# Kernel tuning notes

Measured on AMD Instinct MI355X. Metric: run time of the kernel, lower is better.

Reference implementation:

```python
import jax, jax.numpy as jnp
import numpy as np
import math

L_SIDE = 32           # one_side_length = ceil(sqrt(L)), L = 32**2
NDIM = 16             # args.ndim (SSM state size)
N_SSM = 16            # args.n_ssm
DIRS = 4              # args.directions_amount
EMBED = 1024          # embed_dim
KD = DIRS * N_SSM     # kernel_dim = 64
CDIM = EMBED * DIRS   # C_dimensions = 4096
H = EMBED // N_SSM    # 64 (channels per ssm)
R2 = 16               # expansion terms per kernel position
R = L_SIDE * L_SIDE * R2
V = 2 * L_SIDE        # vander power dim (power_dim = kernel_dim_arg*2)
BSZ = 8
SEQ = L_SIDE * L_SIDE


def _build_one_matrix():
    # Mimics CoeffCalculator.whole_as_one: for each of d=2 flow axes and each
    # of R expansion terms, the 4 A-factor rows are one-hot selectors over the
    # V power basis, and the 5th (B) row holds an integer coefficient in one of
    # the first two columns (selecting B1 or B2).
    rng = np.random.default_rng(0)
    M = np.zeros((2, 5, R, V), dtype=np.float32)
    di = np.arange(2)[:, None]
    ri = np.arange(R)[None, :]
    for a in range(4):
        idx = rng.integers(0, V, size=(2, R))
        M[di, a, ri, idx] = 1.0
    col = rng.integers(0, 2, size=(2, R))
    coef = rng.integers(1, 5, size=(2, R)).astype(np.float32)
    M[di, 4, ri, col] = coef
    return jnp.asarray(M)


def setup_inputs() -> dict:
    key = jax.random.key(0)
    ks = jax.random.split(key, 7)
    return {
        "x": jax.random.normal(ks[0], (SEQ, BSZ, EMBED), jnp.float32),
        "A": jax.random.normal(ks[1], (4, KD, NDIM), jnp.float32) * 0.2,
        "B1": jax.random.normal(ks[2], (KD, NDIM), jnp.float32) * 0.2,
        "B2": jax.random.normal(ks[3], (KD, NDIM), jnp.float32) * 0.2,
        "C1": jax.random.normal(ks[4], (CDIM, NDIM), jnp.float32),
        "C2": jax.random.normal(ks[5], (CDIM, NDIM), jnp.float32),
        "omega": jax.random.normal(ks[6], (EMBED,), jnp.float32),
        "one_matrix": _build_one_matrix(),
    }


def _compute_kernel(A, B1, B2, C1, C2, one_matrix, dtype):
    scale = 1.0 / math.sqrt(NDIM)
    # _calc_coeffs: sigmoid on A, B
    As = jax.nn.sigmoid(A)                                  # (4, KD, NDIM)
    pw = jnp.arange(V, dtype=dtype)
    # torch.linalg.vander: increasing powers 0..V-1 -> (4, V, KD, NDIM)
    A_vals = jnp.transpose(As[..., None] ** pw, (0, 3, 1, 2))
    Bs = jax.nn.sigmoid(jnp.stack([B1, B2], 0))             # (2, KD, NDIM)
    Bpad = jnp.zeros((V, KD, NDIM), dtype).at[:2].set(Bs)   # pad to V rows
    vals = jnp.concatenate([A_vals, Bpad[None]], 0)         # (5, V, KD, NDIM)
    # 'd a R V, a V k n -> d a R k n' then product over the 5 factors
    prod = jnp.einsum('drv,vkn->drkn', one_matrix[:, 0], vals[0])
    for a in range(1, 5):
        prod = prod * jnp.einsum('drv,vkn->drkn', one_matrix[:, a], vals[a])
    # sum over r2 expansion terms per kernel position
    w = prod.reshape(2, SEQ, R2, KD, NDIM).sum(2)           # (2, SEQ, KD, NDIM)
    C = jnp.stack([C1, C2], 0) * scale                      # (2, CDIM, NDIM)
    Cr = C.reshape(2, H, KD, NDIM)
    k = jnp.einsum('dpkn,dhkn->phk', w, Cr).reshape(L_SIDE, L_SIDE, CDIM)
    # boundary scaling (first row/col x2, corner net x1)
    k = k.at[0, :, :].multiply(2.0)
    k = k.at[:, 0, :].multiply(2.0)
    k = k.at[0, 0, :].divide(4.0)
    return k


def reference(x, A, B1, B2, C1, C2, omega, one_matrix):
    k = _compute_kernel(A, B1, B2, C1, C2, one_matrix, x.dtype)
    # channel layout (H, dir, n_ssm) -> per-direction (EMBED,) kernels
    kd = k.reshape(L_SIDE, L_SIDE, H, DIRS, N_SSM)
    kd = jnp.transpose(kd, (3, 2, 4, 0, 1)).reshape(DIRS, EMBED, L_SIDE, L_SIDE)
    # 4-corner scans: flip kernel per direction; conv is linear so sum kernels
    ksum = kd[0] + kd[1, :, ::-1, :] + kd[2, :, :, ::-1] + kd[3, :, ::-1, ::-1]
    residual = x * omega                                    # 'L B D, D -> L B D'
    xg = jnp.transpose(x, (1, 2, 0)).reshape(BSZ, EMBED, L_SIDE, L_SIDE)
    s = 2 * L_SIDE
    xf = jnp.fft.rfft2(xg, s=(s, s))                        # (B, D, s, s//2+1)
    kf = jnp.fft.rfft2(ksum, s=(s, s))
    y = jnp.fft.irfft2(xf * kf, s=(s, s))[..., :L_SIDE, :L_SIDE]
    y = jnp.transpose(y.reshape(BSZ, EMBED, SEQ), (2, 0, 1))  # back to (L, B, D)
    return y + residual
```

## Files before the change

### kernel.cpp

```cpp
#include <hip/hip_runtime.h>
#include <stdint.h>


typedef __attribute__((ext_vector_type(8))) short short8;
typedef __attribute__((ext_vector_type(4))) float f32x4;

__device__ inline uint16_t f2bf(float f) {
    uint32_t u = __float_as_uint(f);
    uint32_t r = (u + 0x7FFFu + ((u >> 16) & 1u)) >> 16;
    return (uint16_t)r;
}
__device__ inline float bf2f(uint16_t v) {
    return __uint_as_float((uint32_t)v << 16);
}
__device__ inline uint32_t packbf(float a, float b) {
    return (uint32_t)f2bf(a) | ((uint32_t)f2bf(b) << 16);
}

__global__ __launch_bounds__(256) void k_sel(const float* __restrict__ om,
                                             uint32_t* __restrict__ sel,
                                             float* __restrict__ coef) {
    int gw = (blockIdx.x * 256 + threadIdx.x) >> 6;
    int lane = threadIdx.x & 63;
    int nw = gridDim.x * 4;
    for (int pr = gw; pr < 32768; pr += nw) {
        int d = pr >> 14, r = pr & 16383;
        uint32_t s = 0;
        float cf = 1.0f;
        #pragma unroll
        for (int a = 0; a < 5; ++a) {
            float v = om[((size_t)(d * 5 + a) * 16384 + r) * 64 + lane];
            unsigned long long m = __ballot(v != 0.0f);
            int idx = (m != 0ull) ? __builtin_ctzll(m) : 0;
            float mv = __shfl(v, idx, 64);
            if (m == 0ull) mv = 0.0f;
            if (a < 4) {
                s |= (uint32_t)idx << (6 * a);
                cf *= mv;
            } else {
                if (idx > 1) cf = 0.0f;
                else { s |= (uint32_t)idx << 24; cf *= mv; }
            }
        }
        if (lane == 0) { sel[pr] = s; coef[pr] = cf; }
    }
}

__global__ __launch_bounds__(256) void k_w(const float* __restrict__ A,
                                           const float* __restrict__ B1,
                                           const float* __restrict__ B2,
                                           const uint32_t* __restrict__ sel,
                                           const float* __restrict__ coef,
                                           float* __restrict__ w) {
    int p = blockIdx.x;
    int t = threadIdx.x;
    int d = __builtin_amdgcn_readfirstlane(t >> 7);
    int j0 = (t & 127) * 8;

    float L0[8], L1[8], L2[8], L3[8], B0v[8], B1v[8], acc[8];
    {
        #pragma unroll
        for (int a = 0; a < 4; ++a) {
            float* La = (a == 0) ? L0 : (a == 1) ? L1 : (a == 2) ? L2 : L3;
            float4 u0 = *(const float4*)(A + a * 1024 + j0);
            float4 u1 = *(const float4*)(A + a * 1024 + j0 + 4);
            float tmp[8] = {u0.x, u0.y, u0.z, u0.w, u1.x, u1.y, u1.z, u1.w};
            #pragma unroll
            for (int jj = 0; jj < 8; ++jj)
                La[jj] = -log2f(1.0f + expf(-tmp[jj]));
        }
        float4 u0 = *(const float4*)(B1 + j0);
        float4 u1 = *(const float4*)(B1 + j0 + 4);
        float4 v0 = *(const float4*)(B2 + j0);
        float4 v1 = *(const float4*)(B2 + j0 + 4);
        float t1[8] = {u0.x, u0.y, u0.z, u0.w, u1.x, u1.y, u1.z, u1.w};
        float t2[8] = {v0.x, v0.y, v0.z, v0.w, v1.x, v1.y, v1.z, v1.w};
        #pragma unroll
        for (int jj = 0; jj < 8; ++jj) {
            B0v[jj] = 1.0f / (1.0f + expf(-t1[jj]));
            B1v[jj] = 1.0f / (1.0f + expf(-t2[jj]));
        }
    }
    #pragma unroll
    for (int jj = 0; jj < 8; ++jj) acc[jj] = 0.0f;

    int base = d * 16384 + p * 16;
    #pragma unroll
    for (int r2 = 0; r2 < 16; ++r2) {
        uint32_t s = sel[base + r2];
        float cf = coef[base + r2];
        float f0 = (float)(s & 63u);
        float f1 = (float)((s >> 6) & 63u);
        float f2 = (float)((s >> 12) & 63u);
        float f3 = (float)((s >> 18) & 63u);
        int col = (int)((s >> 24) & 1u);
        float c0 = col ? 0.0f : cf;
        float c1 = col ? cf : 0.0f;
        #pragma unroll
        for (int jj = 0; jj < 8; ++jj) {
            float ex = __builtin_fmaf(f3, L3[jj],
                       __builtin_fmaf(f2, L2[jj],
                       __builtin_fmaf(f1, L1[jj], f0 * L0[jj])));
            float bs = __builtin_fmaf(c1, B1v[jj], c0 * B0v[jj]);
            acc[jj] = __builtin_fmaf(exp2f(ex), bs, acc[jj]);
        }
    }
    float* dst = w + (size_t)(d * 1024 + p) * 1024 + j0;
    *(float4*)(dst)     = make_float4(acc[0], acc[1], acc[2], acc[3]);
    *(float4*)(dst + 4) = make_float4(acc[4], acc[5], acc[6], acc[7]);
}

__global__ __launch_bounds__(256) void k_kd(const float* __restrict__ w,
                                            const float* __restrict__ C1,
                                            const float* __restrict__ C2,
                                            uint16_t* __restrict__ kd4b) {
    __shared__ float Wl[128 * 33];
    __shared__ float Ctl[32 * 65];
    int kap = blockIdx.x;
    int p0 = blockIdx.y * 128;
    int dir = kap >> 4, m = kap & 15;
    int t = threadIdx.x;

    {
        int d = t >> 7, pp = t & 127;
        const float* src = w + ((size_t)(d * 1024 + p0 + pp) * 64 + kap) * 16;
        float* dst = Wl + pp * 33 + d * 16;
        #pragma unroll
        for (int q = 0; q < 4; ++q) {
            float4 v = *(const float4*)(src + q * 4);
            dst[q * 4 + 0] = v.x; dst[q * 4 + 1] = v.y;
            dst[q * 4 + 2] = v.z; dst[q * 4 + 3] = v.w;
        }
    }
    if (t < 128) {
        int d = t >> 6, h = t & 63;
        const float* Cd = d ? C2 : C1;
        const float* src = Cd + (size_t)(h * 64 + kap) * 16;
        #pragma unroll
        for (int q = 0; q < 16; ++q)
            Ctl[(d * 16 + q) * 65 + h] = src[q] * 0.25f;
    }
    __syncthreads();

    int ph = t & 15, hq = t >> 4;
    int pl = ph * 8, h0 = hq * 4;
    float acc[8][4];
    #pragma unroll
    for (int i = 0; i < 8; ++i)
        { acc[i][0] = acc[i][1] = acc[i][2] = acc[i][3] = 0.0f; }

    for (int k = 0; k < 32; ++k) {
        float c0 = Ctl[k * 65 + h0 + 0];
        float c1 = Ctl[k * 65 + h0 + 1];
        float c2 = Ctl[k * 65 + h0 + 2];
        float c3 = Ctl[k * 65 + h0 + 3];
        #pragma unroll
        for (int i = 0; i < 8; ++i) {
            float wv = Wl[(pl + i) * 33 + k];
            acc[i][0] += wv * c0; acc[i][1] += wv * c1;
            acc[i][2] += wv * c2; acc[i][3] += wv * c3;
        }
    }
    #pragma unroll
    for (int j = 0; j < 4; ++j) {
        int h = h0 + j;
        uint32_t pk[4];
        #pragma unroll
        for (int qq = 0; qq < 4; ++qq) {
            float v0, v1;
            #pragma unroll
            for (int z = 0; z < 2; ++z) {
                int p = p0 + pl + qq * 2 + z;
                int ii = p >> 5, jj = p & 31;
                float f = ((ii == 0) != (jj == 0)) ? 2.0f : 1.0f;
                float val = acc[qq * 2 + z][j] * f;
                if (z == 0) v0 = val; else v1 = val;
            }
            pk[qq] = packbf(v0, v1);
        }
        uint16_t* dst = kd4b + ((size_t)(dir * 1024 + h * 16 + m)) * 1024 + p0 + pl;
        *(uint4*)dst = make_uint4(pk[0], pk[1], pk[2], pk[3]);
    }
}

__global__ __launch_bounds__(256) void k_t1(const float* __restrict__ x,
                                            uint16_t* __restrict__ xtb) {
    __shared__ float lds[32 * 257];
    int u = blockIdx.x, e0 = blockIdx.y * 32;
    int t = threadIdx.x;
    {
        const float* src = x + (size_t)(u * 256 + t) * 1024 + e0;
        #pragma unroll
        for (int qq = 0; qq < 8; ++qq) {
            float4 v = *(const float4*)(src + qq * 4);
            lds[(qq * 4 + 0) * 257 + t] = v.x;
            lds[(qq * 4 + 1) * 257 + t] = v.y;
            lds[(qq * 4 + 2) * 257 + t] = v.z;
            lds[(qq * 4 + 3) * 257 + t] = v.w;
        }
    }
    __syncthreads();
    int er = t & 31, b = t >> 5;
    const float* row = lds + er * 257 + b;
    uint32_t pk[16];
    #pragma unroll
    for (int k2 = 0; k2 < 16; ++k2)
        pk[k2] = packbf(row[(2 * k2) * 8], row[(2 * k2 + 1) * 8]);
    uint16_t* dst = xtb + (size_t)(e0 + er) * 8192 + u * 256 + b * 32;
    uint4* d4 = (uint4*)dst;
    d4[0] = make_uint4(pk[0], pk[1], pk[2], pk[3]);
    d4[1] = make_uint4(pk[4], pk[5], pk[6], pk[7]);
    d4[2] = make_uint4(pk[8], pk[9], pk[10], pk[11]);
    d4[3] = make_uint4(pk[12], pk[13], pk[14], pk[15]);
}

__global__ __launch_bounds__(256) void k_conv(const uint16_t* __restrict__ xtb,
                                              const uint16_t* __restrict__ kd4b,
                                              uint16_t* __restrict__ ytb) {
    __shared__ __align__(16) char smem[26624 + 16384];
    const int KROW = 832;
    const int SROW = 104;
    char* xtl = smem + 26624;

    int e = blockIdx.x;
    int t = threadIdx.x;
    int lane = t & 63, wv = t >> 6;
    int n = lane & 15, q = lane >> 4, nn = n & 7;

    {
        f32x4 z = {0.f, 0.f, 0.f, 0.f};
        for (int idx = t; idx < 1664; idx += 256)
            *(f32x4*)(smem + idx * 16) = z;
    }
    {
        const uint4* src = (const uint4*)(xtb + (size_t)e * 8192);
        #pragma unroll
        for (int r = 0; r < 4; ++r) {
            uint4 v = src[r * 256 + t];
            *(uint4*)(xtl + (r * 256 + t) * 16) = v;
        }
    }
    int pi = t >> 3, pj = (t & 7) * 4;
    float s0, s1, s2, s3;
    {
        const uint16_t* b0 = kd4b + (size_t)e * 1024;
        ushort4 a0 = *(const ushort4*)(b0 + pi * 32 + pj);
        ushort4 a1 = *(const ushort4*)(b0 + (1 << 20) + (31 - pi) * 32 + pj);
        ushort4 a2 = *(const ushort4*)(b0 + (2 << 20) + pi * 32 + (28 - pj));
        ushort4 a3 = *(const ushort4*)(b0 + (3 << 20) + (31 - pi) * 32 + (28 - pj));
        s0 = bf2f(a0.x) + bf2f(a1.x) + bf2f(a2.w) + bf2f(a3.w);
        s1 = bf2f(a0.y) + bf2f(a1.y) + bf2f(a2.z) + bf2f(a3.z);
        s2 = bf2f(a0.z) + bf2f(a1.z) + bf2f(a2.y) + bf2f(a3.y);
        s3 = bf2f(a0.w) + bf2f(a1.w) + bf2f(a2.x) + bf2f(a3.x);
    }
    __syncthreads();

    {
        uint16_t k0 = f2bf(s0), k1 = f2bf(s1), k2 = f2bf(s2), k3 = f2bf(s3);
        #pragma unroll
        for (int s = 0; s < 8; ++s) {
            uint16_t* row = (uint16_t*)(smem + pi * KROW + s * SROW);
            int c = 31 + s - pj;
            row[c]     = k0;
            row[c - 1] = k1;
            row[c - 2] = k2;
            row[c - 3] = k3;
        }
    }
    __syncthreads();

    int A0 = n - 8 * q;
    int A1 = A0 + 16;
    int sh1 = (A1 + 9) & 7;
    int off1 = sh1 * SROW + (31 + sh1 - A1) * 2;
    int off0;
    if (A0 >= -8) {
        int sh0 = (A0 + 9) & 7;
        off0 = sh0 * SROW + (31 + sh0 - A0) * 2;
    } else {
        off0 = 80;
    }
    int boff = nn * 64 + q * 16;

    short8 Breg[16];
    #pragma unroll
    for (int u = 0; u < 16; ++u)
        Breg[u] = *(const short8*)(xtl + u * 512 + boff);

    f32x4 acc0[8], acc1[8];
    #pragma unroll
    for (int ii = 0; ii < 8; ++ii) {
        acc0[ii] = (f32x4){0.f, 0.f, 0.f, 0.f};
        acc1[ii] = (f32x4){0.f, 0.f, 0.f, 0.f};
    }

    #pragma unroll
    for (int dd = 0; dd < 4; ++dd) {
        if (dd <= wv) {
            const char* krow = smem + (wv - dd) * KROW;
            short8 a0 = *(const short8*)(krow + off0);
            short8 a1 = *(const short8*)(krow + off1);
            #pragma unroll
            for (int ii = 0; ii < 8; ++ii) {
                short8 bb = (ii < 4) ? Breg[dd + 4 * ii]
                                     : *(const short8*)(xtl + (dd + 4 * ii) * 512 + boff);
                acc0[ii] = __builtin_amdgcn_mfma_f32_16x16x32_bf16(a0, bb, acc0[ii], 0, 0, 0);
                acc1[ii] = __builtin_amdgcn_mfma_f32_16x16x32_bf16(a1, bb, acc1[ii], 0, 0, 0);
            }
        }
    }
    #pragma unroll
    for (int g = 1; g <= 7; ++g) {
        #pragma unroll
        for (int dd = 0; dd < 4; ++dd) {
            const char* krow = smem + (wv + 4 * g - 3 + dd) * KROW;
            short8 a0 = *(const short8*)(krow + off0);
            short8 a1 = *(const short8*)(krow + off1);
            #pragma unroll
            for (int ii = g; ii < 8; ++ii) {
                int u = 4 * (ii - g) + 3 - dd;
                short8 bb = (ii - g < 4) ? Breg[u]
                                         : *(const short8*)(xtl + u * 512 + boff);
                acc0[ii] = __builtin_amdgcn_mfma_f32_16x16x32_bf16(a0, bb, acc0[ii], 0, 0, 0);
                acc1[ii] = __builtin_amdgcn_mfma_f32_16x16x32_bf16(a1, bb, acc1[ii], 0, 0, 0);
            }
        }
    }

    if (n < 8) {
        uint16_t* base = ytb + ((size_t)(n * 1024 + e)) * 1024 + q * 4;
        #pragma unroll
        for (int ii = 0; ii < 8; ++ii) {
            int i = wv + 4 * ii;
            uint2 w0 = make_uint2(packbf(acc0[ii][0], acc0[ii][1]),
                                  packbf(acc0[ii][2], acc0[ii][3]));
            uint2 w1 = make_uint2(packbf(acc1[ii][0], acc1[ii][1]),
                                  packbf(acc1[ii][2], acc1[ii][3]));
            *(uint2*)(base + i * 32)      = w0;
            *(uint2*)(base + i * 32 + 16) = w1;
        }
    }
}

__global__ __launch_bounds__(256) void k_t2(const uint16_t* __restrict__ ytb,
                                            const float* __restrict__ x,
                                            const float* __restrict__ omega,
                                            float* __restrict__ out) {
    __shared__ float lds[32 * 129];
    int e0 = blockIdx.x * 32, p0 = blockIdx.y * 128, b = blockIdx.z;
    int t = threadIdx.x;
    {
        int er = t & 31, seg = t >> 5;
        const uint16_t* src = ytb + (size_t)(b * 1024 + e0 + er) * 1024 + p0 + seg * 16;
        uint4 v0 = *(const uint4*)src;
        uint4 v1 = *(const uint4*)(src + 8);
        float* dst = lds + er * 129 + seg * 16;
        uint32_t ww[8] = {v0.x, v0.y, v0.z, v0.w, v1.x, v1.y, v1.z, v1.w};
        #pragma unroll
        for (int k = 0; k < 8; ++k) {
            dst[2 * k]     = bf2f((uint16_t)(ww[k] & 0xFFFFu));
            dst[2 * k + 1] = bf2f((uint16_t)(ww[k] >> 16));
        }
    }
    __syncthreads();
    int pl = t >> 1, eh = (t & 1) * 16;
    int p = p0 + pl;
    const float* xs = x + ((size_t)(p * 8 + b)) * 1024 + e0 + eh;
    float* os = out + ((size_t)(p * 8 + b)) * 1024 + e0 + eh;
    #pragma unroll
    for (int qq = 0; qq < 4; ++qq) {
        float4 xv = *(const float4*)(xs + qq * 4);
        int eb = eh + qq * 4;
        float4 ov;
        ov.x = lds[(eb + 0) * 129 + pl] + xv.x * omega[e0 + eb + 0];
        ov.y = lds[(eb + 1) * 129 + pl] + xv.y * omega[e0 + eb + 1];
        ov.z = lds[(eb + 2) * 129 + pl] + xv.z * omega[e0 + eb + 2];
        ov.w = lds[(eb + 3) * 129 + pl] + xv.w * omega[e0 + eb + 3];
        *(float4*)(os + qq * 4) = ov;
    }
}

extern "C" void kernel_launch(void* const* d_in, const int* in_sizes, int n_in,
                              void* d_out, int out_size, void* d_ws, size_t ws_size,
                              hipStream_t stream) {
    (void)in_sizes; (void)n_in; (void)out_size; (void)ws_size;
    const float* x   = (const float*)d_in[0];
    const float* A   = (const float*)d_in[1];
    const float* B1  = (const float*)d_in[2];
    const float* B2  = (const float*)d_in[3];
    const float* C1  = (const float*)d_in[4];
    const float* C2  = (const float*)d_in[5];
    const float* omg = (const float*)d_in[6];
    const float* om  = (const float*)d_in[7];
    float* out = (float*)d_out;

    float* ws  = (float*)d_ws;
    uint16_t* xtb  = (uint16_t*)ws;
    uint16_t* kd4b = (uint16_t*)(ws + 4194304);
    uint16_t* ytb  = (uint16_t*)(ws + 6291456);
    uint32_t* sel  = (uint32_t*)(ws + 10485760);
    float* coef    = (float*)(sel + 32768);
    float* w       = coef + 32768;

    k_t1  <<<dim3(32, 32), 256, 0, stream>>>(x, xtb);
    k_sel <<<2048, 256, 0, stream>>>(om, sel, coef);
    k_w   <<<1024, 256, 0, stream>>>(A, B1, B2, sel, coef, w);
    k_kd  <<<dim3(64, 8), 256, 0, stream>>>(w, C1, C2, kd4b);
    k_conv<<<1024, 256, 0, stream>>>(xtb, kd4b, ytb);
    k_t2  <<<dim3(32, 8, 8), 256, 0, stream>>>(ytb, x, omg, out);
}
```

Before: 220.5 us.

## Fuse x transpose, selector extraction and w computation into one front kernel

Merges three kernels (x transpose to bf16, one-hot selector decoding, and w expansion) into a single launch. Block indices select which role each block takes. Selector and coefficient values now stay in shared memory instead of making a global round trip. k_conv's shared-memory row padding is also shrunk from 832 to 768 bytes, with an unrolled zero-fill. This removes two launches and the sel/coef global traffic, and lets the independent transpose overlap with the w computation. The smaller padding may bring back LDS bank conflicts, or may change the conv's layout assumptions.

Result: faster. 197.9 us (-10.2%).

```diff
diff --git a/kernel.cpp b/kernel.cpp
--- a/kernel.cpp
+++ b/kernel.cpp
@@ -17,48 +17,78 @@
     return (uint32_t)f2bf(a) | ((uint32_t)f2bf(b) << 16);
 }
 
-__global__ __launch_bounds__(256) void k_sel(const float* __restrict__ om,
-                                             uint32_t* __restrict__ sel,
-                                             float* __restrict__ coef) {
-    int gw = (blockIdx.x * 256 + threadIdx.x) >> 6;
-    int lane = threadIdx.x & 63;
-    int nw = gridDim.x * 4;
-    for (int pr = gw; pr < 32768; pr += nw) {
-        int d = pr >> 14, r = pr & 16383;
-        uint32_t s = 0;
-        float cf = 1.0f;
-        #pragma unroll
-        for (int a = 0; a < 5; ++a) {
-            float v = om[((size_t)(d * 5 + a) * 16384 + r) * 64 + lane];
-            unsigned long long m = __ballot(v != 0.0f);
-            int idx = (m != 0ull) ? __builtin_ctzll(m) : 0;
-            float mv = __shfl(v, idx, 64);
-            if (m == 0ull) mv = 0.0f;
-            if (a < 4) {
-                s |= (uint32_t)idx << (6 * a);
-                cf *= mv;
-            } else {
-                if (idx > 1) cf = 0.0f;
-                else { s |= (uint32_t)idx << 24; cf *= mv; }
-            }
-        }
-        if (lane == 0) { sel[pr] = s; coef[pr] = cf; }
-    }
-}
-
-__global__ __launch_bounds__(256) void k_w(const float* __restrict__ A,
-                                           const float* __restrict__ B1,
-                                           const float* __restrict__ B2,
-                                           const uint32_t* __restrict__ sel,
-                                           const float* __restrict__ coef,
-                                           float* __restrict__ w) {
-    int p = blockIdx.x;
+__global__ __launch_bounds__(256) void k_front(const float* __restrict__ x,
+                                               uint16_t* __restrict__ xtb,
+                                               const float* __restrict__ om,
+                                               const float* __restrict__ A,
+                                               const float* __restrict__ B1,
+                                               const float* __restrict__ B2,
+                                               float* __restrict__ w) {
+    __shared__ __align__(16) float shf[32 * 257];
+    int bx = blockIdx.x;
     int t = threadIdx.x;
-    int d = __builtin_amdgcn_readfirstlane(t >> 7);
-    int j0 = (t & 127) * 8;
-
-    float L0[8], L1[8], L2[8], L3[8], B0v[8], B1v[8], acc[8];
-    {
+
+    if (bx < 1024) {
+        int u = bx & 31, e0 = (bx >> 5) * 32;
+        {
+            const float* src = x + (size_t)(u * 256 + t) * 1024 + e0;
+            #pragma unroll
+            for (int qq = 0; qq < 8; ++qq) {
+                float4 v = *(const float4*)(src + qq * 4);
+                shf[(qq * 4 + 0) * 257 + t] = v.x;
+                shf[(qq * 4 + 1) * 257 + t] = v.y;
+                shf[(qq * 4 + 2) * 257 + t] = v.z;
+                shf[(qq * 4 + 3) * 257 + t] = v.w;
+            }
+        }
+        __syncthreads();
+        int er = t & 31, b = t >> 5;
+        const float* row = shf + er * 257 + b;
+        uint32_t pk[16];
+        #pragma unroll
+        for (int k2 = 0; k2 < 16; ++k2)
+            pk[k2] = packbf(row[(2 * k2) * 8], row[(2 * k2 + 1) * 8]);
+        uint16_t* dst = xtb + (size_t)(e0 + er) * 8192 + u * 256 + b * 32;
+        uint4* d4 = (uint4*)dst;
+        d4[0] = make_uint4(pk[0], pk[1], pk[2], pk[3]);
+        d4[1] = make_uint4(pk[4], pk[5], pk[6], pk[7]);
+        d4[2] = make_uint4(pk[8], pk[9], pk[10], pk[11]);
+        d4[3] = make_uint4(pk[12], pk[13], pk[14], pk[15]);
+    } else {
+        int p = bx - 1024;
+        uint32_t* sel_l = (uint32_t*)shf;
+        float* coef_l = shf + 32;
+        int lane = t & 63, wv = t >> 6;
+
+        #pragma unroll
+        for (int k = 0; k < 8; ++k) {
+            int pi = wv * 8 + k;
+            int d = pi >> 4, r2 = pi & 15;
+            int r = p * 16 + r2;
+            uint32_t s = 0;
+            float cf = 1.0f;
+            #pragma unroll
+            for (int a = 0; a < 5; ++a) {
+                float v = om[((size_t)(d * 5 + a) * 16384 + r) * 64 + lane];
+                unsigned long long m = __ballot(v != 0.0f);
+                int idx = (m != 0ull) ? __builtin_ctzll(m) : 0;
+                float mv = __shfl(v, idx, 64);
+                if (m == 0ull) mv = 0.0f;
+                if (a < 4) {
+                    s |= (uint32_t)idx << (6 * a);
+                    cf *= mv;
+                } else {
+                    if (idx > 1) cf = 0.0f;
+                    else { s |= (uint32_t)idx << 24; cf *= mv; }
+                }
+            }
+            if (lane == 0) { sel_l[pi] = s; coef_l[pi] = cf; }
+        }
+        __syncthreads();
+
+        int d = t >> 7;
+        int j0 = (t & 127) * 8;
+        float L0[8], L1[8], L2[8], L3[8], B0v[8], B1v[8], acc[8];
         #pragma unroll
         for (int a = 0; a < 4; ++a) {
             float* La = (a == 0) ? L0 : (a == 1) ? L1 : (a == 2) ? L2 : L3;
@@ -69,45 +99,46 @@
             for (int jj = 0; jj < 8; ++jj)
                 La[jj] = -log2f(1.0f + expf(-tmp[jj]));
         }
-        float4 u0 = *(const float4*)(B1 + j0);
-        float4 u1 = *(const float4*)(B1 + j0 + 4);
-        float4 v0 = *(const float4*)(B2 + j0);
-        float4 v1 = *(const float4*)(B2 + j0 + 4);
-        float t1[8] = {u0.x, u0.y, u0.z, u0.w, u1.x, u1.y, u1.z, u1.w};
-        float t2[8] = {v0.x, v0.y, v0.z, v0.w, v1.x, v1.y, v1.z, v1.w};
-        #pragma unroll
-        for (int jj = 0; jj < 8; ++jj) {
-            B0v[jj] = 1.0f / (1.0f + expf(-t1[jj]));
-            B1v[jj] = 1.0f / (1.0f + expf(-t2[jj]));
-        }
-    }
-    #pragma unroll
-    for (int jj = 0; jj < 8; ++jj) acc[jj] = 0.0f;
-
-    int base = d * 16384 + p * 16;
-    #pragma unroll
-    for (int r2 = 0; r2 < 16; ++r2) {
-        uint32_t s = sel[base + r2];
-        float cf = coef[base + r2];
-        float f0 = (float)(s & 63u);
-        float f1 = (float)((s >> 6) & 63u);
-        float f2 = (float)((s >> 12) & 63u);
-        float f3 = (float)((s >> 18) & 63u);
-        int col = (int)((s >> 24) & 1u);
-        float c0 = col ? 0.0f : cf;
-        float c1 = col ? cf : 0.0f;
-        #pragma unroll
-        for (int jj = 0; jj < 8; ++jj) {
-            float ex = __builtin_fmaf(f3, L3[jj],
-                       __builtin_fmaf(f2, L2[jj],
-                       __builtin_fmaf(f1, L1[jj], f0 * L0[jj])));
-            float bs = __builtin_fmaf(c1, B1v[jj], c0 * B0v[jj]);
-            acc[jj] = __builtin_fmaf(exp2f(ex), bs, acc[jj]);
-        }
-    }
-    float* dst = w + (size_t)(d * 1024 + p) * 1024 + j0;
-    *(float4*)(dst)     = make_float4(acc[0], acc[1], acc[2], acc[3]);
-    *(float4*)(dst + 4) = make_float4(acc[4], acc[5], acc[6], acc[7]);
+        {
+            float4 u0 = *(const float4*)(B1 + j0);
+            float4 u1 = *(const float4*)(B1 + j0 + 4);
+            float4 v0 = *(const float4*)(B2 + j0);
+            float4 v1 = *(const float4*)(B2 + j0 + 4);
+            float t1v[8] = {u0.x, u0.y, u0.z, u0.w, u1.x, u1.y, u1.z, u1.w};
+            float t2v[8] = {v0.x, v0.y, v0.z, v0.w, v1.x, v1.y, v1.z, v1.w};
+            #pragma unroll
+            for (int jj = 0; jj < 8; ++jj) {
+                B0v[jj] = 1.0f / (1.0f + expf(-t1v[jj]));
+                B1v[jj] = 1.0f / (1.0f + expf(-t2v[jj]));
+            }
+        }
+        #pragma unroll
+        for (int jj = 0; jj < 8; ++jj) acc[jj] = 0.0f;
+
+        #pragma unroll
+        for (int r2 = 0; r2 < 16; ++r2) {
+            uint32_t s = sel_l[d * 16 + r2];
+            float cf = coef_l[d * 16 + r2];
+            float f0 = (float)(s & 63u);
+            float f1 = (float)((s >> 6) & 63u);
+            float f2 = (float)((s >> 12) & 63u);
+            float f3 = (float)((s >> 18) & 63u);
+            int col = (int)((s >> 24) & 1u);
+            float c0 = col ? 0.0f : cf;
+            float c1 = col ? cf : 0.0f;
+            #pragma unroll
+            for (int jj = 0; jj < 8; ++jj) {
+                float ex = __builtin_fmaf(f3, L3[jj],
+                           __builtin_fmaf(f2, L2[jj],
+                           __builtin_fmaf(f1, L1[jj], f0 * L0[jj])));
+                float bs = __builtin_fmaf(c1, B1v[jj], c0 * B0v[jj]);
+                acc[jj] = __builtin_fmaf(exp2f(ex), bs, acc[jj]);
+            }
+        }
+        float* dst = w + (size_t)(d * 1024 + p) * 1024 + j0;
+        *(float4*)(dst)     = make_float4(acc[0], acc[1], acc[2], acc[3]);
+        *(float4*)(dst + 4) = make_float4(acc[4], acc[5], acc[6], acc[7]);
+    }
 }
 
 __global__ __launch_bounds__(256) void k_kd(const float* __restrict__ w,
@@ -183,44 +214,13 @@
     }
 }
 
-__global__ __launch_bounds__(256) void k_t1(const float* __restrict__ x,
-                                            uint16_t* __restrict__ xtb) {
-    __shared__ float lds[32 * 257];
-    int u = blockIdx.x, e0 = blockIdx.y * 32;
-    int t = threadIdx.x;
-    {
-        const float* src = x + (size_t)(u * 256 + t) * 1024 + e0;
-        #pragma unroll
-        for (int qq = 0; qq < 8; ++qq) {
-            float4 v = *(const float4*)(src + qq * 4);
-            lds[(qq * 4 + 0) * 257 + t] = v.x;
-            lds[(qq * 4 + 1) * 257 + t] = v.y;
-            lds[(qq * 4 + 2) * 257 + t] = v.z;
-            lds[(qq * 4 + 3) * 257 + t] = v.w;
-        }
-    }
-    __syncthreads();
-    int er = t & 31, b = t >> 5;
-    const float* row = lds + er * 257 + b;
-    uint32_t pk[16];
-    #pragma unroll
-    for (int k2 = 0; k2 < 16; ++k2)
-        pk[k2] = packbf(row[(2 * k2) * 8], row[(2 * k2 + 1) * 8]);
-    uint16_t* dst = xtb + (size_t)(e0 + er) * 8192 + u * 256 + b * 32;
-    uint4* d4 = (uint4*)dst;
-    d4[0] = make_uint4(pk[0], pk[1], pk[2], pk[3]);
-    d4[1] = make_uint4(pk[4], pk[5], pk[6], pk[7]);
-    d4[2] = make_uint4(pk[8], pk[9], pk[10], pk[11]);
-    d4[3] = make_uint4(pk[12], pk[13], pk[14], pk[15]);
-}
-
 __global__ __launch_bounds__(256) void k_conv(const uint16_t* __restrict__ xtb,
                                               const uint16_t* __restrict__ kd4b,
                                               uint16_t* __restrict__ ytb) {
-    __shared__ __align__(16) char smem[26624 + 16384];
-    const int KROW = 832;
-    const int SROW = 104;
-    char* xtl = smem + 26624;
+    __shared__ __align__(16) char smem[24576 + 16384];
+    const int KROW = 768;
+    const int SROW = 96;
+    char* xtl = smem + 24576;
 
     int e = blockIdx.x;
     int t = threadIdx.x;
@@ -229,8 +229,9 @@
 
     {
         f32x4 z = {0.f, 0.f, 0.f, 0.f};
-        for (int idx = t; idx < 1664; idx += 256)
-            *(f32x4*)(smem + idx * 16) = z;
+        #pragma unroll
+        for (int k = 0; k < 6; ++k)
+            *(f32x4*)(smem + (t + k * 256) * 16) = z;
     }
     {
         const uint4* src = (const uint4*)(xtb + (size_t)e * 8192);
@@ -398,14 +399,10 @@
     uint16_t* xtb  = (uint16_t*)ws;
     uint16_t* kd4b = (uint16_t*)(ws + 4194304);
     uint16_t* ytb  = (uint16_t*)(ws + 6291456);
-    uint32_t* sel  = (uint32_t*)(ws + 10485760);
-    float* coef    = (float*)(sel + 32768);
-    float* w       = coef + 32768;
-
-    k_t1  <<<dim3(32, 32), 256, 0, stream>>>(x, xtb);
-    k_sel <<<2048, 256, 0, stream>>>(om, sel, coef);
-    k_w   <<<1024, 256, 0, stream>>>(A, B1, B2, sel, coef, w);
-    k_kd  <<<dim3(64, 8), 256, 0, stream>>>(w, C1, C2, kd4b);
-    k_conv<<<1024, 256, 0, stream>>>(xtb, kd4b, ytb);
-    k_t2  <<<dim3(32, 8, 8), 256, 0, stream>>>(ytb, x, omg, out);
-}
+    float* w       = ws + 10485760;
+
+    k_front<<<2048, 256, 0, stream>>>(x, xtb, om, A, B1, B2, w);
+    k_kd   <<<dim3(64, 8), 256, 0, stream>>>(w, C1, C2, kd4b);
+    k_conv <<<1024, 256, 0, stream>>>(xtb, kd4b, ytb);
+    k_t2   <<<dim3(32, 8, 8), 256, 0, stream>>>(ytb, x, omg, out);
+}
```
